# Kernel optimization log

Measured on AMD Instinct MI355X. Metric: run time of the kernel, lower is better.

## Reference

```python
import jax, jax.numpy as jnp
import numpy as np

B, C, H, W = 2048, 6, 128, 96
OUT_H, OUT_W = 32, 24  # PIL resize((24, 32)) -> width=24, height=32

def setup_inputs() -> dict:
    key = jax.random.key(0)
    kx, ky = jax.random.split(key)
    x = jax.random.normal(kx, (B, C, H, W), dtype=jnp.float32)
    y = jax.random.randint(ky, (B,), 0, 10, dtype=jnp.int32)  # unused by forward
    return {"x": x, "y": y}

def reference(x, y):
    # Batched bilinear resize of every (batch, channel) image from (H, W) to (32, 24).
    # antialias=True matches PIL's BILINEAR triangle filter with scaled support
    # when downsampling. Batch/channel dims keep their size -> identity along them.
    resized = jax.image.resize(
        x, (x.shape[0], x.shape[1], OUT_H, OUT_W), method="bilinear", antialias=True
    ).astype(jnp.float32)
    # view(-1, 6, 768): each channel's 32*24 map flattens to a 768-dim feature.
    return resized.reshape(-1, 6, OUT_H * OUT_W)
```

## Files before the change

### kernel.cpp

```cpp
#include <hip/hip_runtime.h>


#define IMG_H 128
#define IMG_W 96
#define ROUT_H 32
#define ROUT_W 24
#define LDSTRIDE 100
#define MIDSTRIDE 25

__global__ __launch_bounds__(256, 2)
void resize_aa_kernel(const float* __restrict__ x, float* __restrict__ out) {
    __shared__ float s_in[IMG_H * LDSTRIDE];
    __shared__ float s_mid[IMG_H * MIDSTRIDE];

    const int img = blockIdx.x;
    const int tid = threadIdx.x;
    const float* __restrict__ src = x + (size_t)img * (IMG_H * IMG_W);

    const float4* __restrict__ src4 = (const float4*)src;
#pragma unroll
    for (int k = 0; k < 12; ++k) {
        int f = tid + k * 256;
        float4 g = src4[f];
        int row = f / 24;
        int c   = f - row * 24;
        *(float4*)(&s_in[row * LDSTRIDE + 4 * c]) = g;
    }
    __syncthreads();

    {
        int r = tid & 127;
        int h = tid >> 7;
        const float* rowp = &s_in[r * LDSTRIDE];
        int c0 = 12 * h;

        float4 prev = (h == 0) ? make_float4(0.f, 0.f, 0.f, 0.f)
                               : *(const float4*)(rowp + 4 * (c0 - 1));
        float4 cur  = *(const float4*)(rowp + 4 * c0);
#pragma unroll
        for (int j = 0; j < 12; ++j) {
            int ow = c0 + j;
            float4 next = (ow + 1 < ROUT_W) ? *(const float4*)(rowp + 4 * (ow + 1))
                                            : make_float4(0.f, 0.f, 0.f, 0.f);
            float w0 = 1.f/32, w1 = 3.f/32, w2 = 5.f/32, w3 = 7.f/32,
                  w4 = 7.f/32, w5 = 5.f/32, w6 = 3.f/32, w7 = 1.f/32;
            if (ow == 0) {
                const float s = 1.0f / 3.5f;
                w0 = 0.f;        w1 = 0.f;
                w2 = 0.625f * s; w3 = 0.875f * s; w4 = 0.875f * s;
                w5 = 0.625f * s; w6 = 0.375f * s; w7 = 0.125f * s;
            } else if (ow == ROUT_W - 1) {
                const float s = 1.0f / 3.5f;
                w0 = 0.125f * s; w1 = 0.375f * s; w2 = 0.625f * s;
                w3 = 0.875f * s; w4 = 0.875f * s; w5 = 0.625f * s;
                w6 = 0.f;        w7 = 0.f;
            }
            float acc = w0 * prev.z + w1 * prev.w
                      + w2 * cur.x  + w3 * cur.y + w4 * cur.z + w5 * cur.w
                      + w6 * next.x + w7 * next.y;
            s_mid[r * MIDSTRIDE + ow] = acc;
            prev = cur; cur = next;
        }
    }
    __syncthreads();

    float* __restrict__ dst = out + (size_t)img * (ROUT_H * ROUT_W);
#pragma unroll
    for (int k = 0; k < 3; ++k) {
        int idx = tid + k * 256;
        int oh = idx / ROUT_W;
        int ow = idx - oh * ROUT_W;
        int r0 = 4 * oh - 2;

        float w[8] = {1.f/32, 3.f/32, 5.f/32, 7.f/32, 7.f/32, 5.f/32, 3.f/32, 1.f/32};
        if (oh == 0) {
            const float s = 1.0f / 3.5f;
            w[0] = 0.f;        w[1] = 0.f;
            w[2] = 0.625f * s; w[3] = 0.875f * s; w[4] = 0.875f * s;
            w[5] = 0.625f * s; w[6] = 0.375f * s; w[7] = 0.125f * s;
        } else if (oh == ROUT_H - 1) {
            const float s = 1.0f / 3.5f;
            w[0] = 0.125f * s; w[1] = 0.375f * s; w[2] = 0.625f * s;
            w[3] = 0.875f * s; w[4] = 0.875f * s; w[5] = 0.625f * s;
            w[6] = 0.f;        w[7] = 0.f;
        }
        float acc = 0.f;
#pragma unroll
        for (int t = 0; t < 8; ++t) {
            int r = r0 + t;
            r = r < 0 ? 0 : (r > IMG_H - 1 ? IMG_H - 1 : r);
            acc += w[t] * s_mid[r * MIDSTRIDE + ow];
        }
        dst[idx] = acc;
    }
}

extern "C" void kernel_launch(void* const* d_in, const int* in_sizes, int n_in,
                              void* d_out, int out_size, void* d_ws, size_t ws_size,
                              hipStream_t stream) {
    const float* x = (const float*)d_in[0];
    float* out = (float*)d_out;
    const int n_img = 2048 * 6;
    resize_aa_kernel<<<n_img, 256, 0, stream>>>(x, out);
}
```

Baseline: 764.1 us.

## Do vertical pass first straight from global memory, drop input LDS staging

Measured after the change: 765.7 us. No clear change (+0.2%).

```diff
diff --git a/kernel.cpp b/kernel.cpp
--- a/kernel.cpp
+++ b/kernel.cpp
@@ -3,94 +3,86 @@
 
 #define IMG_H 128
 #define IMG_W 96
+#define IN_W4 24
 #define ROUT_H 32
 #define ROUT_W 24
-#define LDSTRIDE 100
-#define MIDSTRIDE 25
+#define MSTRIDE 100
 
-__global__ __launch_bounds__(256, 2)
+__global__ __launch_bounds__(256, 4)
 void resize_aa_kernel(const float* __restrict__ x, float* __restrict__ out) {
-    __shared__ float s_in[IMG_H * LDSTRIDE];
-    __shared__ float s_mid[IMG_H * MIDSTRIDE];
+    __shared__ float s_mid[ROUT_H * MSTRIDE];
 
     const int img = blockIdx.x;
     const int tid = threadIdx.x;
-    const float* __restrict__ src = x + (size_t)img * (IMG_H * IMG_W);
+    const float4* __restrict__ src4 =
+        (const float4*)(x + (size_t)img * (IMG_H * IMG_W));
 
-    const float4* __restrict__ src4 = (const float4*)src;
 #pragma unroll
-    for (int k = 0; k < 12; ++k) {
-        int f = tid + k * 256;
-        float4 g = src4[f];
-        int row = f / 24;
-        int c   = f - row * 24;
-        *(float4*)(&s_in[row * LDSTRIDE + 4 * c]) = g;
-    }
-    __syncthreads();
+    for (int k = 0; k < 3; ++k) {
+        const int idx = tid + k * 256;
+        const int oh  = idx / IN_W4;
+        const int c4  = idx - oh * IN_W4;
+        const int r0  = 4 * oh - 2;
 
-    {
-        int r = tid & 127;
-        int h = tid >> 7;
-        const float* rowp = &s_in[r * LDSTRIDE];
-        int c0 = 12 * h;
+        float w0 = 1.f/32, w1 = 3.f/32, w2 = 5.f/32, w3 = 7.f/32,
+              w4 = 7.f/32, w5 = 5.f/32, w6 = 3.f/32, w7 = 1.f/32;
+        if (oh == 0) {
+            const float s = 1.0f / 3.5f;
+            w0 = 0.f;        w1 = 0.f;
+            w2 = 0.625f * s; w3 = 0.875f * s; w4 = 0.875f * s;
+            w5 = 0.625f * s; w6 = 0.375f * s; w7 = 0.125f * s;
+        } else if (oh == ROUT_H - 1) {
+            const float s = 1.0f / 3.5f;
+            w0 = 0.125f * s; w1 = 0.375f * s; w2 = 0.625f * s;
+            w3 = 0.875f * s; w4 = 0.875f * s; w5 = 0.625f * s;
+            w6 = 0.f;        w7 = 0.f;
+        }
+        const float wt[8] = {w0, w1, w2, w3, w4, w5, w6, w7};
 
-        float4 prev = (h == 0) ? make_float4(0.f, 0.f, 0.f, 0.f)
-                               : *(const float4*)(rowp + 4 * (c0 - 1));
-        float4 cur  = *(const float4*)(rowp + 4 * c0);
+        float4 acc = make_float4(0.f, 0.f, 0.f, 0.f);
 #pragma unroll
-        for (int j = 0; j < 12; ++j) {
-            int ow = c0 + j;
-            float4 next = (ow + 1 < ROUT_W) ? *(const float4*)(rowp + 4 * (ow + 1))
-                                            : make_float4(0.f, 0.f, 0.f, 0.f);
-            float w0 = 1.f/32, w1 = 3.f/32, w2 = 5.f/32, w3 = 7.f/32,
-                  w4 = 7.f/32, w5 = 5.f/32, w6 = 3.f/32, w7 = 1.f/32;
-            if (ow == 0) {
-                const float s = 1.0f / 3.5f;
-                w0 = 0.f;        w1 = 0.f;
-                w2 = 0.625f * s; w3 = 0.875f * s; w4 = 0.875f * s;
-                w5 = 0.625f * s; w6 = 0.375f * s; w7 = 0.125f * s;
-            } else if (ow == ROUT_W - 1) {
-                const float s = 1.0f / 3.5f;
-                w0 = 0.125f * s; w1 = 0.375f * s; w2 = 0.625f * s;
-                w3 = 0.875f * s; w4 = 0.875f * s; w5 = 0.625f * s;
-                w6 = 0.f;        w7 = 0.f;
-            }
-            float acc = w0 * prev.z + w1 * prev.w
-                      + w2 * cur.x  + w3 * cur.y + w4 * cur.z + w5 * cur.w
-                      + w6 * next.x + w7 * next.y;
-            s_mid[r * MIDSTRIDE + ow] = acc;
-            prev = cur; cur = next;
+        for (int t = 0; t < 8; ++t) {
+            int r = r0 + t;
+            r = r < 0 ? 0 : (r > IMG_H - 1 ? IMG_H - 1 : r);
+            float4 v = src4[r * IN_W4 + c4];
+            acc.x += wt[t] * v.x; acc.y += wt[t] * v.y;
+            acc.z += wt[t] * v.z; acc.w += wt[t] * v.w;
         }
+        *(float4*)(&s_mid[oh * MSTRIDE + 4 * c4]) = acc;
     }
     __syncthreads();
 
     float* __restrict__ dst = out + (size_t)img * (ROUT_H * ROUT_W);
 #pragma unroll
     for (int k = 0; k < 3; ++k) {
-        int idx = tid + k * 256;
-        int oh = idx / ROUT_W;
-        int ow = idx - oh * ROUT_W;
-        int r0 = 4 * oh - 2;
+        const int idx = tid + k * 256;
+        const int oh  = idx / ROUT_W;
+        const int ow  = idx - oh * ROUT_W;
+        const float* rowp = &s_mid[oh * MSTRIDE];
 
-        float w[8] = {1.f/32, 3.f/32, 5.f/32, 7.f/32, 7.f/32, 5.f/32, 3.f/32, 1.f/32};
-        if (oh == 0) {
+        const int pi = (ow > 0)          ? ow - 1 : 0;
+        const int ni = (ow < ROUT_W - 1) ? ow + 1 : ROUT_W - 1;
+        const float4 prev = *(const float4*)(rowp + 4 * pi);
+        const float4 cur  = *(const float4*)(rowp + 4 * ow);
+        const float4 next = *(const float4*)(rowp + 4 * ni);
+
+        float w0 = 1.f/32, w1 = 3.f/32, w2 = 5.f/32, w3 = 7.f/32,
+              w4 = 7.f/32, w5 = 5.f/32, w6 = 3.f/32, w7 = 1.f/32;
+        if (ow == 0) {
             const float s = 1.0f / 3.5f;
-            w[0] = 0.f;        w[1] = 0.f;
-            w[2] = 0.625f * s; w[3] = 0.875f * s; w[4] = 0.875f * s;
-            w[5] = 0.625f * s; w[6] = 0.375f * s; w[7] = 0.125f * s;
-        } else if (oh == ROUT_H - 1) {
+            w0 = 0.f;        w1 = 0.f;
+            w2 = 0.625f * s; w3 = 0.875f * s; w4 = 0.875f * s;
+            w5 = 0.625f * s; w6 = 0.375f * s; w7 = 0.125f * s;
+        } else if (ow == ROUT_W - 1) {
             const float s = 1.0f / 3.5f;
-            w[0] = 0.125f * s; w[1] = 0.375f * s; w[2] = 0.625f * s;
-            w[3] = 0.875f * s; w[4] = 0.875f * s; w[5] = 0.625f * s;
-            w[6] = 0.f;        w[7] = 0.f;
+            w0 = 0.125f * s; w1 = 0.375f * s; w2 = 0.625f * s;
+            w3 = 0.875f * s; w4 = 0.875f * s; w5 = 0.625f * s;
+            w6 = 0.f;        w7 = 0.f;
         }
-        float acc = 0.f;
-#pragma unroll
-        for (int t = 0; t < 8; ++t) {
-            int r = r0 + t;
-            r = r < 0 ? 0 : (r > IMG_H - 1 ? IMG_H - 1 : r);
-            acc += w[t] * s_mid[r * MIDSTRIDE + ow];
-        }
+
+        const float acc = w0 * prev.z + w1 * prev.w
+                        + w2 * cur.x  + w3 * cur.y + w4 * cur.z + w5 * cur.w
+                        + w6 * next.x + w7 * next.y;
         dst[idx] = acc;
     }
 }
```
